# Optimization experiments

Hardware: AMD Instinct MI355X
Metric: run time of the kernel (lower is better)

## Reference

```python
import jax, jax.numpy as jnp
import numpy as np

HIDDEN_DIM = 64  # self.hidden_dim = inc
N = 16384
C = 64


def setup_inputs() -> dict:
    key = jax.random.key(0)
    k1, k2, k3, k4, k5 = jax.random.split(key, 5)
    scale = 1.0 / np.sqrt(C)
    return {
        "hidden": jax.random.normal(k1, (N, C), dtype=jnp.float32),
        "query": jax.random.normal(k2, (N, C), dtype=jnp.float32),
        "Wq": jax.random.normal(k3, (C, C), dtype=jnp.float32) * scale,
        "Wk": jax.random.normal(k4, (C, C), dtype=jnp.float32) * scale,
        "Wv": jax.random.normal(k5, (C, C), dtype=jnp.float32) * scale,
    }


def reference(hidden, query, Wq, Wk, Wv):
    # Per-voxel linear projections (center-tap of the sparse 3x3x3 convs)
    q = query @ Wq            # [Nq, C]
    k = hidden @ Wk           # [Nk, C]
    v = hidden @ Wv           # [Nk, C]
    # score = q @ k.T / sqrt(hidden_dim)
    score = jnp.einsum("qc,kc->qk", q, k) / jnp.sqrt(jnp.float32(HIDDEN_DIM))
    attn = jax.nn.softmax(score, axis=-1)  # [Nq, Nk]
    weight = attn @ v         # [Nq, C] -> new hidden.F
    return weight
```

## Files before the change

### kernel.cpp

```cpp
#include <hip/hip_runtime.h>
#include <hip/hip_bf16.h>

#define NT 16384
#define CD 64

typedef __attribute__((ext_vector_type(8))) short bf16x8;
typedef __attribute__((ext_vector_type(16))) float f32x16;
typedef __attribute__((ext_vector_type(2))) int int2v;

#define AS1 __attribute__((address_space(1)))
#define AS3 __attribute__((address_space(3)))

__global__ __launch_bounds__(256) void proj_kernel(
    const float* __restrict__ hidden, const float* __restrict__ query,
    const float* __restrict__ Wq, const float* __restrict__ Wk, const float* __restrict__ Wv,
    __hip_bfloat16* __restrict__ qb, __hip_bfloat16* __restrict__ kb,
    __hip_bfloat16* __restrict__ vTb)
{
    __shared__ float qin[32][64];
    __shared__ float hin[32][64];
    const int tid = threadIdx.x;
    const int R0 = blockIdx.x * 32;
    {
        int r = tid >> 3, c0 = (tid & 7) * 8;
        const float4* qs = (const float4*)(query + (size_t)(R0 + r) * CD + c0);
        const float4* hs = (const float4*)(hidden + (size_t)(R0 + r) * CD + c0);
        *(float4*)&qin[r][c0]     = qs[0];
        *(float4*)&qin[r][c0 + 4] = qs[1];
        *(float4*)&hin[r][c0]     = hs[0];
        *(float4*)&hin[r][c0 + 4] = hs[1];
    }
    __syncthreads();
    const int c = tid & 63, rg = tid >> 6;
    const float SC = 0.18033688011112042f;
    float aq[8] = {0.f}, ak[8] = {0.f}, av[8] = {0.f};
    #pragma unroll 4
    for (int j = 0; j < 64; ++j) {
        float wq = Wq[j * 64 + c], wk = Wk[j * 64 + c], wv = Wv[j * 64 + c];
        #pragma unroll
        for (int r8 = 0; r8 < 8; ++r8) {
            float qv = qin[rg * 8 + r8][j];
            float hv = hin[rg * 8 + r8][j];
            aq[r8] += qv * wq;
            ak[r8] += hv * wk;
            av[r8] += hv * wv;
        }
    }
    #pragma unroll
    for (int r8 = 0; r8 < 8; ++r8) {
        int row = R0 + rg * 8 + r8;
        qb[(size_t)row * CD + c] = __float2bfloat16(aq[r8] * SC);
        kb[(size_t)row * CD + c] = __float2bfloat16(ak[r8]);
    }
    union { bf16x8 v; __hip_bfloat16 h[8]; } u;
    #pragma unroll
    for (int r8 = 0; r8 < 8; ++r8) u.h[r8] = __float2bfloat16(av[r8]);
    *(bf16x8*)(vTb + (size_t)c * NT + R0 + rg * 8) = u.v;
}

__device__ __forceinline__ void stage_tiles(
    char* kdst, char* vdst,
    const __hip_bfloat16* kb, const __hip_bfloat16* vTb,
    int kv, int wid, int lane)
{
    const char* kt = (const char*)(kb + (size_t)kv * CD);
    #pragma unroll
    for (int j = 0; j < 2; ++j) {
        int ob = (wid * 2 + j) * 1024;
        int o  = ob + lane * 16;
        int so = o ^ (((o >> 7) & 7) << 4);
        __builtin_amdgcn_global_load_lds((const AS1 void*)(kt + so),
                                         (AS3 void*)(kdst + ob), 16, 0, 0);
    }
    #pragma unroll
    for (int j = 0; j < 2; ++j) {
        int ob = (wid * 2 + j) * 1024;
        int o  = ob + lane * 16;
        int c  = o >> 7;
        int colb = (o & 127) ^ ((c & 7) << 4);
        __builtin_amdgcn_global_load_lds(
            (const AS1 void*)((const char*)vTb + ((size_t)c * NT + kv) * 2 + colb),
            (AS3 void*)(vdst + ob), 16, 0, 0);
    }
}

__device__ __forceinline__ void softpack_half(
    const f32x16& s, float& lsum, int paw[2][4])
{
    float p[16];
    #pragma unroll
    for (int r = 0; r < 16; ++r) p[r] = __builtin_amdgcn_exp2f(s[r]);
    {
        float t0 = ((p[0] + p[1]) + (p[2] + p[3])) + ((p[4] + p[5]) + (p[6] + p[7]));
        float t1 = ((p[8] + p[9]) + (p[10] + p[11])) + ((p[12] + p[13]) + (p[14] + p[15]));
        lsum += t0 + t1;
    }
    int w[8];
    #pragma unroll
    for (int r2 = 0; r2 < 4; ++r2)
        #pragma unroll
        for (int u = 0; u < 2; ++u)
            asm("v_cvt_pk_bf16_f32 %0, %1, %2"
                : "=v"(w[r2 * 2 + u]) : "v"(p[4*r2 + 2*u]), "v"(p[4*r2 + 2*u + 1]));
    #pragma unroll
    for (int r2e = 0; r2e < 4; r2e += 2)
        #pragma unroll
        for (int u = 0; u < 2; ++u) {
            int2v ra = __builtin_amdgcn_permlane32_swap(w[r2e*2 + u], w[(r2e+1)*2 + u], false, false);
            paw[r2e >> 1][u]     = ra.x;
            paw[r2e >> 1][2 + u] = ra.y;
        }
}

__global__ __launch_bounds__(256, 4) void flash_kernel(
    const __hip_bfloat16* __restrict__ qb, const __hip_bfloat16* __restrict__ kb,
    const __hip_bfloat16* __restrict__ vTb,
    __hip_bfloat16* __restrict__ part, float* __restrict__ lbuf, float* __restrict__ out,
    int nsplit, int kvlen)
{
    __shared__ __align__(16) char kbuf[2][8192];
    __shared__ __align__(16) char vbuf[2][8192];

    const int tid  = threadIdx.x;
    const int lane = tid & 63, wid = tid >> 6;
    const int l31 = lane & 31, h = lane >> 5;
    const int split = blockIdx.x % nsplit;
    const int qblk  = blockIdx.x / nsplit;
    const int q0  = qblk * 128 + wid * 32;
    const int kv0 = split * kvlen;
    const int ntile = kvlen / 64;

    bf16x8 Qf[4];
    #pragma unroll
    for (int cc = 0; cc < 4; ++cc)
        Qf[cc] = *(const bf16x8*)(qb + (size_t)(q0 + l31) * CD + cc * 16 + h * 8);

    f32x16 acc[2];
    #pragma unroll
    for (int dt = 0; dt < 2; ++dt)
        #pragma unroll
        for (int r = 0; r < 16; ++r) acc[dt][r] = 0.f;
    float lsum = 0.f;

    const int krow0 = l31, krow1 = 32 + l31;
    const int kswz  = (l31 & 7) << 4;

    stage_tiles(kbuf[0], vbuf[0], kb, vTb, kv0, wid, lane);
    asm volatile("s_waitcnt vmcnt(0)" ::: "memory");
    __syncthreads();

    for (int t = 0; t < ntile; ++t) {
        const int b = t & 1;
        if (t + 1 < ntile)
            stage_tiles(kbuf[b ^ 1], vbuf[b ^ 1], kb, vTb, kv0 + (t + 1) * 64, wid, lane);

        f32x16 s0, s1;
        #pragma unroll
        for (int r = 0; r < 16; ++r) { s0[r] = 0.f; s1[r] = 0.f; }
        __builtin_amdgcn_s_setprio(1);
        #pragma unroll
        for (int cc = 0; cc < 4; ++cc) {
            int colb = (cc * 32 + h * 16) ^ kswz;
            bf16x8 k0 = *(const bf16x8*)(kbuf[b] + krow0 * 128 + colb);
            bf16x8 k1 = *(const bf16x8*)(kbuf[b] + krow1 * 128 + colb);
            s0 = __builtin_amdgcn_mfma_f32_32x32x16_bf16(k0, Qf[cc], s0, 0, 0, 0);
            s1 = __builtin_amdgcn_mfma_f32_32x32x16_bf16(k1, Qf[cc], s1, 0, 0, 0);
        }
        __builtin_amdgcn_s_setprio(0);

        int pa[2][4], pb[2][4];
        softpack_half(s0, lsum, pa);
        softpack_half(s1, lsum, pb);

        __builtin_amdgcn_s_setprio(1);
        #pragma unroll
        for (int kc = 0; kc < 4; ++kc) {
            int colb = (kc * 32 + h * 16) ^ kswz;
            bf16x8 v0 = *(const bf16x8*)(vbuf[b] + krow0 * 128 + colb);
            bf16x8 v1 = *(const bf16x8*)(vbuf[b] + krow1 * 128 + colb);
            union { int i[4]; bf16x8 v; } pu;
            #pragma unroll
            for (int j = 0; j < 4; ++j) pu.i[j] = (kc < 2) ? pa[kc][j] : pb[kc - 2][j];
            acc[0] = __builtin_amdgcn_mfma_f32_32x32x16_bf16(pu.v, v0, acc[0], 0, 0, 0);
            acc[1] = __builtin_amdgcn_mfma_f32_32x32x16_bf16(pu.v, v1, acc[1], 0, 0, 0);
        }
        __builtin_amdgcn_s_setprio(0);

        asm volatile("s_waitcnt vmcnt(0)" ::: "memory");
        __syncthreads();
    }

    float lfull = lsum + __shfl_xor(lsum, 32);

    if (nsplit == 1) {
        #pragma unroll
        for (int dt = 0; dt < 2; ++dt)
            #pragma unroll
            for (int r = 0; r < 16; ++r) {
                int qrow = (r & 3) + 8 * (r >> 2) + 4 * h;
                int li = __builtin_amdgcn_ds_bpermute(qrow * 4, __float_as_int(lfull));
                out[(size_t)(q0 + qrow) * CD + dt * 32 + l31] =
                    acc[dt][r] * __builtin_amdgcn_rcpf(__int_as_float(li));
            }
    } else {
        __hip_bfloat16* pb2 = part + ((size_t)split * NT + q0) * CD;
        #pragma unroll
        for (int dt = 0; dt < 2; ++dt)
            #pragma unroll
            for (int r = 0; r < 16; ++r) {
                int qrow = (r & 3) + 8 * (r >> 2) + 4 * h;
                pb2[qrow * CD + dt * 32 + l31] = __float2bfloat16(acc[dt][r]);
            }
        if (h == 0)
            lbuf[(size_t)split * NT + q0 + l31] = lfull;
    }
}

__global__ __launch_bounds__(256) void combine_kernel(
    const __hip_bfloat16* __restrict__ part, const float* __restrict__ lbuf,
    float* __restrict__ out, int S)
{
    const int tid = threadIdx.x;
    const int row = blockIdx.x * 4 + (tid >> 6);
    const int c = tid & 63;
    float L = 0.f, o = 0.f;
    for (int s = 0; s < S; ++s) {
        L += lbuf[(size_t)s * NT + row];
        o += __bfloat162float(part[((size_t)s * NT + row) * CD + c]);
    }
    out[(size_t)row * CD + c] = o / L;
}

extern "C" void kernel_launch(void* const* d_in, const int* in_sizes, int n_in,
                              void* d_out, int out_size, void* d_ws, size_t ws_size,
                              hipStream_t stream)
{
    (void)in_sizes; (void)n_in; (void)out_size;
    const float* hidden = (const float*)d_in[0];
    const float* query  = (const float*)d_in[1];
    const float* Wq = (const float*)d_in[2];
    const float* Wk = (const float*)d_in[3];
    const float* Wv = (const float*)d_in[4];
    float* out = (float*)d_out;

    char* ws = (char*)d_ws;
    __hip_bfloat16* qb  = (__hip_bfloat16*)ws;
    __hip_bfloat16* kb  = qb + (size_t)NT * CD;
    __hip_bfloat16* vTb = kb + (size_t)NT * CD;
    const size_t base = (size_t)3 * NT * CD * 2;
    const size_t per  = (size_t)NT * CD * 2 + (size_t)NT * 4;

    int S = 1;
    if (ws_size >= base + 16 * per) S = 16;
    else if (ws_size >= base + 8 * per) S = 8;
    else if (ws_size >= base + 4 * per) S = 4;
    else if (ws_size >= base + 2 * per) S = 2;

    __hip_bfloat16* part = (__hip_bfloat16*)(ws + base);
    float* lbuf = (float*)(ws + base + (size_t)S * NT * CD * 2);

    hipLaunchKernelGGL(proj_kernel, dim3(NT / 32), dim3(256), 0, stream,
                       hidden, query, Wq, Wk, Wv, qb, kb, vTb);
    hipLaunchKernelGGL(flash_kernel, dim3((NT / 128) * S), dim3(256), 0, stream,
                       qb, kb, vTb, part, lbuf, out, S, NT / S);
    if (S > 1)
        hipLaunchKernelGGL(combine_kernel, dim3(NT / 4), dim3(256), 0, stream,
                           part, lbuf, out, S);
}
```

Before: 109.8 us.

## Store V in MFMA-fragment-ordered tiles and read K/V LDS without swizzle

Result: no change. 109.4 us (-0.3%).

```diff
diff --git a/kernel.cpp b/kernel.cpp
--- a/kernel.cpp
+++ b/kernel.cpp
@@ -15,7 +15,7 @@
     const float* __restrict__ hidden, const float* __restrict__ query,
     const float* __restrict__ Wq, const float* __restrict__ Wk, const float* __restrict__ Wv,
     __hip_bfloat16* __restrict__ qb, __hip_bfloat16* __restrict__ kb,
-    __hip_bfloat16* __restrict__ vTb)
+    __hip_bfloat16* __restrict__ vcb)
 {
     __shared__ float qin[32][64];
     __shared__ float hin[32][64];
@@ -55,31 +55,35 @@
     union { bf16x8 v; __hip_bfloat16 h[8]; } u;
     #pragma unroll
     for (int r8 = 0; r8 < 8; ++r8) u.h[r8] = __float2bfloat16(av[r8]);
-    *(bf16x8*)(vTb + (size_t)c * NT + R0 + rg * 8) = u.v;
+    {
+        int kb0 = R0 + rg * 8;
+        __hip_bfloat16* dst = vcb + (size_t)(kb0 >> 6) * 4096
+                              + (((kb0 >> 4) & 3) * 1024) + c * 16 + ((kb0 >> 3) & 1) * 8;
+        *(bf16x8*)dst = u.v;
+    }
 }
 
 __device__ __forceinline__ void stage_tiles(
     char* kdst, char* vdst,
-    const __hip_bfloat16* kb, const __hip_bfloat16* vTb,
+    const __hip_bfloat16* kb, const __hip_bfloat16* vcb,
     int kv, int wid, int lane)
 {
     const char* kt = (const char*)(kb + (size_t)kv * CD);
+    const char* vt = (const char*)vcb + (size_t)(kv >> 6) * 8192;
     #pragma unroll
     for (int j = 0; j < 2; ++j) {
         int ob = (wid * 2 + j) * 1024;
         int o  = ob + lane * 16;
-        int so = o ^ (((o >> 7) & 7) << 4);
-        __builtin_amdgcn_global_load_lds((const AS1 void*)(kt + so),
-                                         (AS3 void*)(kdst + ob), 16, 0, 0);
+        int cc = o >> 11, key = (o >> 5) & 63, h1 = (o >> 4) & 1;
+        __builtin_amdgcn_global_load_lds(
+            (const AS1 void*)(kt + key * 128 + cc * 32 + h1 * 16),
+            (AS3 void*)(kdst + ob), 16, 0, 0);
     }
     #pragma unroll
     for (int j = 0; j < 2; ++j) {
         int ob = (wid * 2 + j) * 1024;
-        int o  = ob + lane * 16;
-        int c  = o >> 7;
-        int colb = (o & 127) ^ ((c & 7) << 4);
         __builtin_amdgcn_global_load_lds(
-            (const AS1 void*)((const char*)vTb + ((size_t)c * NT + kv) * 2 + colb),
+            (const AS1 void*)(vt + ob + lane * 16),
             (AS3 void*)(vdst + ob), 16, 0, 0);
     }
 }
@@ -114,7 +118,7 @@
 
 __global__ __launch_bounds__(256, 4) void flash_kernel(
     const __hip_bfloat16* __restrict__ qb, const __hip_bfloat16* __restrict__ kb,
-    const __hip_bfloat16* __restrict__ vTb,
+    const __hip_bfloat16* __restrict__ vcb,
     __hip_bfloat16* __restrict__ part, float* __restrict__ lbuf, float* __restrict__ out,
     int nsplit, int kvlen)
 {
@@ -142,17 +146,17 @@
         for (int r = 0; r < 16; ++r) acc[dt][r] = 0.f;
     float lsum = 0.f;
 
-    const int krow0 = l31, krow1 = 32 + l31;
-    const int kswz  = (l31 & 7) << 4;
-
-    stage_tiles(kbuf[0], vbuf[0], kb, vTb, kv0, wid, lane);
+    const int ro0 = l31 * 32 + h * 16;
+    const int ro1 = (32 + l31) * 32 + h * 16;
+
+    stage_tiles(kbuf[0], vbuf[0], kb, vcb, kv0, wid, lane);
     asm volatile("s_waitcnt vmcnt(0)" ::: "memory");
     __syncthreads();
 
     for (int t = 0; t < ntile; ++t) {
         const int b = t & 1;
         if (t + 1 < ntile)
-            stage_tiles(kbuf[b ^ 1], vbuf[b ^ 1], kb, vTb, kv0 + (t + 1) * 64, wid, lane);
+            stage_tiles(kbuf[b ^ 1], vbuf[b ^ 1], kb, vcb, kv0 + (t + 1) * 64, wid, lane);
 
         f32x16 s0, s1;
         #pragma unroll
@@ -160,9 +164,8 @@
         __builtin_amdgcn_s_setprio(1);
         #pragma unroll
         for (int cc = 0; cc < 4; ++cc) {
-            int colb = (cc * 32 + h * 16) ^ kswz;
-            bf16x8 k0 = *(const bf16x8*)(kbuf[b] + krow0 * 128 + colb);
-            bf16x8 k1 = *(const bf16x8*)(kbuf[b] + krow1 * 128 + colb);
+            bf16x8 k0 = *(const bf16x8*)(kbuf[b] + cc * 2048 + ro0);
+            bf16x8 k1 = *(const bf16x8*)(kbuf[b] + cc * 2048 + ro1);
             s0 = __builtin_amdgcn_mfma_f32_32x32x16_bf16(k0, Qf[cc], s0, 0, 0, 0);
             s1 = __builtin_amdgcn_mfma_f32_32x32x16_bf16(k1, Qf[cc], s1, 0, 0, 0);
         }
@@ -175,9 +178,8 @@
         __builtin_amdgcn_s_setprio(1);
         #pragma unroll
         for (int kc = 0; kc < 4; ++kc) {
-            int colb = (kc * 32 + h * 16) ^ kswz;
-            bf16x8 v0 = *(const bf16x8*)(vbuf[b] + krow0 * 128 + colb);
-            bf16x8 v1 = *(const bf16x8*)(vbuf[b] + krow1 * 128 + colb);
+            bf16x8 v0 = *(const bf16x8*)(vbuf[b] + kc * 2048 + ro0);
+            bf16x8 v1 = *(const bf16x8*)(vbuf[b] + kc * 2048 + ro1);
             union { int i[4]; bf16x8 v; } pu;
             #pragma unroll
             for (int j = 0; j < 4; ++j) pu.i[j] = (kc < 2) ? pa[kc][j] : pb[kc - 2][j];
@@ -246,7 +248,7 @@
     char* ws = (char*)d_ws;
     __hip_bfloat16* qb  = (__hip_bfloat16*)ws;
     __hip_bfloat16* kb  = qb + (size_t)NT * CD;
-    __hip_bfloat16* vTb = kb + (size_t)NT * CD;
+    __hip_bfloat16* vcb = kb + (size_t)NT * CD;
     const size_t base = (size_t)3 * NT * CD * 2;
     const size_t per  = (size_t)NT * CD * 2 + (size_t)NT * 4;
 
@@ -260,9 +262,9 @@
     float* lbuf = (float*)(ws + base + (size_t)S * NT * CD * 2);
 
     hipLaunchKernelGGL(proj_kernel, dim3(NT / 32), dim3(256), 0, stream,
-                       hidden, query, Wq, Wk, Wv, qb, kb, vTb);
+                       hidden, query, Wq, Wk, Wv, qb, kb, vcb);
     hipLaunchKernelGGL(flash_kernel, dim3((NT / 128) * S), dim3(256), 0, stream,
-                       qb, kb, vTb, part, lbuf, out, S, NT / S);
+                       qb, kb, vcb, part, lbuf, out, S, NT / S);
     if (S > 1)
         hipLaunchKernelGGL(combine_kernel, dim3(NT / 4), dim3(256), 0, stream,
                            part, lbuf, out, S);
```
